# Kernel tuning notes

Measured on AMD Instinct MI355X. Metric: run time of the kernel, lower is better.

The kernel has to match this reference:

```python
import jax, jax.numpy as jnp
import numpy as np

INPUT_DIM = 41      # observed channels
D = 2 * INPUT_DIM   # attention value dim (values + mask concat)
E = 128             # embed_time
NH = 1              # num_heads
DK = E // NH
H = 128             # nhidden
NLIN = 50
LAT = 20
B, TK, TQ = 8, 512, 128


def _lin_init(k, out_d, in_d):
    return jax.random.normal(k, (out_d, in_d)) * (1.0 / np.sqrt(in_d))


def setup_inputs() -> dict:
    key = jax.random.key(0)
    ks = jax.random.split(key, 32)
    vals = jax.random.normal(ks[0], (B, TK, INPUT_DIM))
    obs = (jax.random.uniform(ks[1], (B, TK, INPUT_DIM)) > 0.3).astype(jnp.float32)
    x = jnp.concatenate([vals * obs, obs], axis=-1)          # [B,TK,2*INPUT_DIM]
    time_steps = jnp.sort(jax.random.uniform(ks[2], (B, TK)), axis=1)
    query = jnp.linspace(0.0, 1.0, TQ)                        # reference time points
    inp = dict(x=x, time_steps=time_steps, query=query)
    # learned time embedders (mtan_time_embedder): Linear(1,1) + Linear(1,E-1)
    inp['e1_wp'] = jax.random.normal(ks[3], (E - 1,)); inp['e1_bp'] = jax.random.normal(ks[4], (E - 1,)) * 0.1
    inp['e1_wl'] = jax.random.normal(ks[5], (1,));     inp['e1_bl'] = jax.random.normal(ks[6], (1,)) * 0.1
    inp['e2_wp'] = jax.random.normal(ks[7], (E - 1,)); inp['e2_bp'] = jax.random.normal(ks[8], (E - 1,)) * 0.1
    inp['e2_wl'] = jax.random.normal(ks[9], (1,));     inp['e2_bl'] = jax.random.normal(ks[10], (1,)) * 0.1
    # multiTimeAttention linears
    inp['Wq'] = _lin_init(ks[11], E, E); inp['bq'] = jnp.zeros((E,))
    inp['Wk'] = _lin_init(ks[12], E, E); inp['bk'] = jnp.zeros((E,))
    inp['Wo'] = _lin_init(ks[13], H, NH * D); inp['bo'] = jnp.zeros((H,))
    # bidirectional GRU (PyTorch layout: W_ih [3H,in], W_hh [3H,H])
    inp['gwi_f'] = _lin_init(ks[14], 3 * H, H); inp['gwh_f'] = _lin_init(ks[15], 3 * H, H)
    inp['gbi_f'] = jnp.zeros((3 * H,));         inp['gbh_f'] = jnp.zeros((3 * H,))
    inp['gwi_b'] = _lin_init(ks[16], 3 * H, H); inp['gwh_b'] = _lin_init(ks[17], 3 * H, H)
    inp['gbi_b'] = jnp.zeros((3 * H,));         inp['gbh_b'] = jnp.zeros((3 * H,))
    # hiddens_to_z0 MLP
    inp['W1'] = _lin_init(ks[18], NLIN, 2 * H); inp['b1'] = jnp.zeros((NLIN,))
    inp['W2'] = _lin_init(ks[19], 2 * LAT, NLIN); inp['b2'] = jnp.zeros((2 * LAT,))
    return inp


def _time_embed(tt, wp, bp, wl, bl):
    tt = tt[..., None]                               # [...,1]
    out1 = tt * wl + bl                              # [...,1]
    out2 = jnp.sin(tt * wp + bp)                     # [...,E-1]
    return jnp.concatenate([out1, out2], axis=-1)    # [...,E]


def _gru_scan(xs, Wi, Wh, bi, bh):
    # xs: [T,B,in] -> hidden states [T,B,H]; PyTorch GRU equations
    h0 = jnp.zeros((xs.shape[1], Wh.shape[1]), xs.dtype)
    def step(h, xt):
        gi = xt @ Wi.T + bi
        gh = h @ Wh.T + bh
        ir, iz, inn = jnp.split(gi, 3, axis=-1)
        hr, hz, hn = jnp.split(gh, 3, axis=-1)
        r = jax.nn.sigmoid(ir + hr)
        z = jax.nn.sigmoid(iz + hz)
        n = jnp.tanh(inn + r * hn)
        hnew = (1.0 - z) * n + z * h
        return hnew, hnew
    _, ys = jax.lax.scan(step, h0, xs)
    return ys


def reference(x, time_steps, query, e1_wp, e1_bp, e1_wl, e1_bl, e2_wp, e2_bp, e2_wl, e2_bl,
              Wq, bq, Wk, bk, Wo, bo, gwi_f, gwh_f, gbi_f, gbh_f, gwi_b, gwh_b, gbi_b, gbh_b,
              W1, b1, W2, b2):
    b, tk, _ = x.shape
    tq = query.shape[0]
    mask = x[:, :, INPUT_DIM:]                                 # [B,TK,INPUT_DIM]
    mask2 = jnp.concatenate([mask, mask], axis=-1)             # [B,TK,D]
    k_emb = _time_embed(time_steps, e1_wp, e1_bp, e1_wl, e1_bl)   # embedder1(key)   [B,TK,E]
    q_emb = _time_embed(query[None, :], e2_wp, e2_bp, e2_wl, e2_bl)  # embedder2(query) [1,TQ,E]
    q = (q_emb @ Wq.T + bq).reshape(1, tq, NH, DK).transpose(0, 2, 1, 3)   # [1,h,TQ,dk]
    k = (k_emb @ Wk.T + bk).reshape(b, tk, NH, DK).transpose(0, 2, 1, 3)   # [B,h,TK,dk]
    scores = jnp.einsum('ahqd,bhkd->bhqk', q, k) / np.sqrt(DK)             # [B,h,TQ,TK]
    # per-channel masked softmax over keys (the blown-up 5D tensor in the original)
    s5 = jnp.where(mask2[:, None, None, :, :] == 0, -1e9, scores[..., None])  # [B,h,TQ,TK,D]
    p = jax.nn.softmax(s5, axis=-2)
    att = jnp.einsum('bhqkd,bkd->bhqd', p, x)                  # value = x; [B,h,TQ,D]
    att = att.transpose(0, 2, 1, 3).reshape(b, tq, NH * D)
    out = att @ Wo.T + bo                                      # [B,TQ,H]
    xs = out.transpose(1, 0, 2)                                # [TQ,B,H]
    hf = _gru_scan(xs, gwi_f, gwh_f, gbi_f, gbh_f)
    hb = _gru_scan(xs[::-1], gwi_b, gwh_b, gbi_b, gbh_b)[::-1]
    h = jnp.concatenate([hf, hb], axis=-1).transpose(1, 0, 2)  # [B,TQ,2H]
    z = jax.nn.relu(h @ W1.T + b1) @ W2.T + b2                 # [B,TQ,2*LAT]
    return z
```

## Files before the change

kernel.cpp:

```cpp
#include <hip/hip_runtime.h>
#include <math.h>

#define TKK 512
#define TQQ 128
#define BB  8
#define EE  128
#define DD  82
#define IND 41
#define HH  128
#define G3  384
#define NL  50
#define OD  40

typedef __attribute__((ext_vector_type(8))) short short8v;
typedef __attribute__((ext_vector_type(4))) float f32x4;
#define MFMA16(a, b, c) __builtin_amdgcn_mfma_f32_16x16x32_bf16(a, b, c, 0, 0, 0)
#define RCP(x) __builtin_amdgcn_rcpf(x)

__device__ __forceinline__ short f2bf(float f) {
  unsigned u = __float_as_uint(f);
  unsigned r = (u + 0x7fffu + ((u >> 16) & 1u)) >> 16;
  return (short)r;
}
__device__ __forceinline__ float dot4(float4 a, float4 b) {
  return a.x * b.x + a.y * b.y + a.z * b.z + a.w * b.w;
}

__global__ __launch_bounds__(128) void embed_project(
    const float* __restrict__ time_steps, const float* __restrict__ query,
    const float* __restrict__ e1_wp, const float* __restrict__ e1_bp,
    const float* __restrict__ e1_wl, const float* __restrict__ e1_bl,
    const float* __restrict__ e2_wp, const float* __restrict__ e2_bp,
    const float* __restrict__ e2_wl, const float* __restrict__ e2_bl,
    const float* __restrict__ Wk, const float* __restrict__ bk,
    const float* __restrict__ Wq, const float* __restrict__ bq,
    float* __restrict__ kproj, float* __restrict__ qproj) {
  __shared__ float emb[8][EE];
  int i = blockIdx.x;
  int e = threadIdx.x;
  const float *wp, *bp, *wl, *bl, *W, *bias;
  float* out;
  int row0;
  const float* tsrc;
  if (i < 512) {
    int b = i & 7, rg = i >> 3;
    row0 = b * TKK + rg * 8;
    tsrc = time_steps + row0;
    wp = e1_wp; bp = e1_bp; wl = e1_wl; bl = e1_bl; W = Wk; bias = bk;
    out = kproj + (size_t)row0 * EE;
  } else {
    int qg = i - 512;
    row0 = qg * 8;
    tsrc = query + row0;
    wp = e2_wp; bp = e2_bp; wl = e2_wl; bl = e2_bl; W = Wq; bias = bq;
    out = qproj + (size_t)row0 * EE;
  }
  float wpv = 0.f, bpv = 0.f;
  if (e > 0) { wpv = wp[e - 1]; bpv = bp[e - 1]; }
  float wlv = wl[0], blv = bl[0];
#pragma unroll
  for (int r = 0; r < 8; r++) {
    float t = tsrc[r];
    emb[r][e] = (e == 0) ? (t * wlv + blv) : sinf(t * wpv + bpv);
  }
  __syncthreads();
  const float4* wr4 = (const float4*)(W + (size_t)e * EE);
  const float4* em4 = (const float4*)emb;
  float bv = bias[e];
  float acc[8];
#pragma unroll
  for (int r = 0; r < 8; r++) acc[r] = bv;
#pragma unroll 4
  for (int c = 0; c < 32; c++) {
    float4 wv = wr4[c];
#pragma unroll
    for (int r = 0; r < 8; r++) acc[r] += dot4(wv, em4[r * 32 + c]);
  }
#pragma unroll
  for (int r = 0; r < 8; r++) out[(size_t)r * EE + e] = acc[r];
}

__global__ __launch_bounds__(512) void attention(
    const float* __restrict__ x, const float* __restrict__ kproj,
    const float* __restrict__ qproj, const float* __restrict__ Wo,
    const float* __restrict__ bo,
    const float* __restrict__ gwi_f, const float* __restrict__ gbi_f,
    const float* __restrict__ gwi_b, const float* __restrict__ gbi_b,
    float* __restrict__ gi) {
  __shared__ float qv[4][EE];
  __shared__ float4 w4[TKK];
  __shared__ float red[8][4];
  __shared__ float mfin[4];
  __shared__ float part[4][4][DD];
  __shared__ float numb[4][DD];
  __shared__ float attb[4][DD];
  __shared__ float xsr[4][EE];
  __shared__ float wo_lds[HH * DD];
  int b = blockIdx.x & 7, qg = blockIdx.x >> 3;
  int q0 = qg * 4;
  int tid = threadIdx.x;
  int rq = tid >> 2, ec = tid & 3;

  {
    qv[tid >> 7][tid & 127] = qproj[(size_t)(q0 + (tid >> 7)) * EE + (tid & 127)];
    const float4* wo4 = (const float4*)Wo;
    float4* wl4 = (float4*)wo_lds;
#pragma unroll
    for (int it = 0; it < 6; it++) {
      int i4 = tid + it * 512;
      if (i4 < HH * DD / 4) wl4[i4] = wo4[i4];
    }
  }
  __syncthreads();

  const float scale = 0.08838834764831845f;
  float lm[4] = {-1e30f, -1e30f, -1e30f, -1e30f};
  const float4* qv4 = (const float4*)qv;
  for (int p = 0; p < 4; p++) {
    int r = p * 128 + rq;
    const float4* kr = (const float4*)(kproj + (size_t)(b * TKK + r) * EE);
    float s[4] = {0.f, 0.f, 0.f, 0.f};
#pragma unroll
    for (int c = 0; c < 8; c++) {
      float4 kv = kr[c * 4 + ec];
#pragma unroll
      for (int qi = 0; qi < 4; qi++) s[qi] += dot4(kv, qv4[qi * 32 + c * 4 + ec]);
    }
#pragma unroll
    for (int qi = 0; qi < 4; qi++) {
      s[qi] += __shfl_xor(s[qi], 1, 64);
      s[qi] += __shfl_xor(s[qi], 2, 64);
      s[qi] *= scale;
      lm[qi] = fmaxf(lm[qi], s[qi]);
    }
    if (ec == 0) { float4 sv = {s[0], s[1], s[2], s[3]}; w4[r] = sv; }
  }
  for (int off = 32; off; off >>= 1)
#pragma unroll
    for (int qi = 0; qi < 4; qi++) lm[qi] = fmaxf(lm[qi], __shfl_xor(lm[qi], off, 64));
  if ((tid & 63) == 0)
#pragma unroll
    for (int qi = 0; qi < 4; qi++) red[tid >> 6][qi] = lm[qi];
  __syncthreads();
  if (tid < 4) {
    float m = red[0][tid];
#pragma unroll
    for (int w = 1; w < 8; w++) m = fmaxf(m, red[w][tid]);
    mfin[tid] = m;
  }
  __syncthreads();
  {
    float m0 = mfin[0], m1 = mfin[1], m2 = mfin[2], m3 = mfin[3];
    float4 v0 = w4[tid];
    v0.x = __expf(v0.x - m0); v0.y = __expf(v0.y - m1);
    v0.z = __expf(v0.z - m2); v0.w = __expf(v0.w - m3);
    w4[tid] = v0;
  }
  __syncthreads();

  {
    int c2 = tid >> 7, d = tid & 127;
    if (d < DD) {
      const float* xp = x + ((size_t)(b * TKK + c2 * 128)) * DD + d;
      float a0 = 0.f, a1 = 0.f, a2 = 0.f, a3 = 0.f;
#pragma unroll 8
      for (int k = 0; k < 128; k++) {
        float xv = xp[(size_t)k * DD];
        float4 wv = w4[c2 * 128 + k];
        a0 += wv.x * xv; a1 += wv.y * xv; a2 += wv.z * xv; a3 += wv.w * xv;
      }
      part[c2][0][d] = a0; part[c2][1][d] = a1; part[c2][2][d] = a2; part[c2][3][d] = a3;
    }
  }
  __syncthreads();
  if (tid < DD) {
#pragma unroll
    for (int qi = 0; qi < 4; qi++)
      numb[qi][tid] = part[0][qi][tid] + part[1][qi][tid] + part[2][qi][tid] + part[3][qi][tid];
  }
  __syncthreads();
  if (tid < DD) {
    int j = tid % IND;
#pragma unroll
    for (int qi = 0; qi < 4; qi++)
      attb[qi][tid] = numb[qi][tid] * RCP(numb[qi][IND + j]);
  }
  __syncthreads();

  {
    int o = tid & 127, g = tid >> 7;
    const float* wrow = wo_lds + o * DD;
    float acc = bo[o];
#pragma unroll 2
    for (int d = 0; d < DD; d++) acc += wrow[d] * attb[g][d];
    xsr[g][o] = acc;
  }
  __syncthreads();

  const float4* xs4 = (const float4*)xsr;
  for (int p = 0; p < 6; p++) {
    int o = p * 128 + rq;
    int dirn = (o >= G3) ? 1 : 0;
    int oo = o - dirn * G3;
    int gate = oo >> 7, col = oo & 127;
    const float4* wr = (const float4*)((dirn ? gwi_b : gwi_f) + (size_t)oo * EE);
    float a[4] = {0.f, 0.f, 0.f, 0.f};
#pragma unroll
    for (int c = 0; c < 8; c++) {
      float4 wv = wr[c * 4 + ec];
#pragma unroll
      for (int qi = 0; qi < 4; qi++) a[qi] += dot4(wv, xs4[qi * 32 + c * 4 + ec]);
    }
#pragma unroll
    for (int qi = 0; qi < 4; qi++) {
      a[qi] += __shfl_xor(a[qi], 1, 64);
      a[qi] += __shfl_xor(a[qi], 2, 64);
    }
    float bi = (dirn ? gbi_b : gbi_f)[oo];
    if (ec == 0) {
      float* gp = gi + (((size_t)(dirn * BB + b) * TQQ + q0) * HH + col) * 4 + gate;
      gp[0] = a[0] + bi; gp[512] = a[1] + bi; gp[1024] = a[2] + bi; gp[1536] = a[3] + bi;
    }
  }
}

__global__ __launch_bounds__(256, 1) void gru_seq(const float* __restrict__ gi,
                                                  const float* __restrict__ gwh_f,
                                                  const float* __restrict__ gbh_f,
                                                  const float* __restrict__ gwh_b,
                                                  const float* __restrict__ gbh_b,
                                                  float* __restrict__ hcat) {
  __shared__ short hb[2][HH];
  int dir = blockIdx.x >> 3, b = blockIdx.x & 7;
  const float* Wh = dir ? gwh_b : gwh_f;
  const float* bh = dir ? gbh_b : gbh_f;
  int tid = threadIdx.x;
  int w = tid >> 6, l = tid & 63;
  int lhi = l >> 4, llo = l & 15;
  int col0 = 32 * w + llo, col1 = col0 + 16;
  bool c0 = (lhi < 2);
  int o_sel = c0 ? col0 : col1;
  bool wr_lane = ((lhi & 1) == 0);

  if (tid < HH) { hb[0][tid] = 0; hb[1][tid] = 0; }

  short8v Bf[2][3][4];
#pragma unroll
  for (int tj = 0; tj < 2; tj++) {
    int colt = 32 * w + 16 * tj + llo;
#pragma unroll
    for (int g = 0; g < 3; g++) {
      const float* wrp = Wh + (size_t)(g * HH + colt) * EE;
#pragma unroll
      for (int kk = 0; kk < 4; kk++) {
        int k0 = kk * 32 + lhi * 8;
        short8v v;
#pragma unroll
        for (int i = 0; i < 8; i++) v[i] = f2bf(wrp[k0 + i]);
        Bf[tj][g][kk] = v;
      }
    }
  }
  float bhr = bh[o_sel], bhz = bh[HH + o_sel], bhn = bh[2 * HH + o_sel];
  float hprev = 0.f;
  float hst[16];

  float4 g0, g1, g2, g3;
  const size_t dbase = ((size_t)(dir * BB + b) * TQQ) * 512 + (size_t)o_sel * 4;

  auto gi_load = [&](int step, float4& dst) {
    int tt = dir ? (TQQ - 1 - step) : step;
    dst = *(const float4*)(gi + dbase + (size_t)tt * 512);
  };
  __syncthreads();
  gi_load(0, g0); gi_load(1, g1); gi_load(2, g2);

  auto body = [&](int step, float4& gc, float4& gn, float& hs) {
    int cur = step & 1;
    const char* hrow = (const char*)&hb[cur][0];
    int ao = lhi * 16;
    short8v A0 = *(const short8v*)(hrow + 0 * 64 + ao);
    short8v A1 = *(const short8v*)(hrow + 1 * 64 + ao);
    short8v A2 = *(const short8v*)(hrow + 2 * 64 + ao);
    short8v A3 = *(const short8v*)(hrow + 3 * 64 + ao);
    { int ls = step + 3; gi_load(ls > TQQ - 1 ? TQQ - 1 : ls, gn); }
    f32x4 z4 = {0.f, 0.f, 0.f, 0.f};
    f32x4 aR0 = z4, aZ0 = z4, aN0 = z4, aR1 = z4, aZ1 = z4, aN1 = z4;
    aR0 = MFMA16(A0, Bf[0][0][0], aR0); aZ0 = MFMA16(A0, Bf[0][1][0], aZ0); aN0 = MFMA16(A0, Bf[0][2][0], aN0);
    aR1 = MFMA16(A0, Bf[1][0][0], aR1); aZ1 = MFMA16(A0, Bf[1][1][0], aZ1); aN1 = MFMA16(A0, Bf[1][2][0], aN1);
    aR0 = MFMA16(A1, Bf[0][0][1], aR0); aZ0 = MFMA16(A1, Bf[0][1][1], aZ0); aN0 = MFMA16(A1, Bf[0][2][1], aN0);
    aR1 = MFMA16(A1, Bf[1][0][1], aR1); aZ1 = MFMA16(A1, Bf[1][1][1], aZ1); aN1 = MFMA16(A1, Bf[1][2][1], aN1);
    aR0 = MFMA16(A2, Bf[0][0][2], aR0); aZ0 = MFMA16(A2, Bf[0][1][2], aZ0); aN0 = MFMA16(A2, Bf[0][2][2], aN0);
    aR1 = MFMA16(A2, Bf[1][0][2], aR1); aZ1 = MFMA16(A2, Bf[1][1][2], aZ1); aN1 = MFMA16(A2, Bf[1][2][2], aN1);
    aR0 = MFMA16(A3, Bf[0][0][3], aR0); aZ0 = MFMA16(A3, Bf[0][1][3], aZ0); aN0 = MFMA16(A3, Bf[0][2][3], aN0);
    aR1 = MFMA16(A3, Bf[1][0][3], aR1); aZ1 = MFMA16(A3, Bf[1][1][3], aZ1); aN1 = MFMA16(A3, Bf[1][2][3], aN1);
    float rs = c0 ? aR0[0] : aR1[0];
    float zs = c0 ? aZ0[0] : aZ1[0];
    float ns = c0 ? aN0[0] : aN1[0];
    float rp = gc.x + bhr + rs;
    float zp = gc.y + bhz + zs;
    float hn = ns + bhn;
    float r = RCP(1.f + __expf(-rp));
    float z = RCP(1.f + __expf(-zp));
    float a = gc.z + r * hn;
    float e = __expf(2.f * a);
    float n = 1.f - 2.f * RCP(1.f + e);
    float hnew = n + z * (hprev - n);
    hprev = hnew;
    hs = hnew;
    if (wr_lane) hb[cur ^ 1][o_sel] = f2bf(hnew);
    asm volatile("s_waitcnt lgkmcnt(0)" ::: "memory");
    __builtin_amdgcn_s_barrier();
    __builtin_amdgcn_sched_barrier(0);
  };

  for (int so = 0; so < TQQ / 16; so++) {
    int s0i = so * 16;
    body(s0i + 0,  g0, g3, hst[0]);
    body(s0i + 1,  g1, g0, hst[1]);
    body(s0i + 2,  g2, g1, hst[2]);
    body(s0i + 3,  g3, g2, hst[3]);
    body(s0i + 4,  g0, g3, hst[4]);
    body(s0i + 5,  g1, g0, hst[5]);
    body(s0i + 6,  g2, g1, hst[6]);
    body(s0i + 7,  g3, g2, hst[7]);
    body(s0i + 8,  g0, g3, hst[8]);
    body(s0i + 9,  g1, g0, hst[9]);
    body(s0i + 10, g2, g1, hst[10]);
    body(s0i + 11, g3, g2, hst[11]);
    body(s0i + 12, g0, g3, hst[12]);
    body(s0i + 13, g1, g0, hst[13]);
    body(s0i + 14, g2, g1, hst[14]);
    body(s0i + 15, g3, g2, hst[15]);
    if (wr_lane) {
#pragma unroll
      for (int si = 0; si < 16; si++) {
        int step = s0i + si;
        int t = dir ? (TQQ - 1 - step) : step;
        hcat[((size_t)b * TQQ + t) * (2 * HH) + dir * HH + o_sel] = hst[si];
      }
    }
  }
}

__global__ __launch_bounds__(512) void mlp_out(const float* __restrict__ hcat,
                                               const float* __restrict__ W1,
                                               const float* __restrict__ b1,
                                               const float* __restrict__ W2,
                                               const float* __restrict__ b2,
                                               float* __restrict__ out) {
  __shared__ float hrow[8][2 * HH];
  __shared__ float ybuf[8][52];
  int i = blockIdx.x;
  int b = i & 7, tg = i >> 3;
  int tid = threadIdx.x;
  size_t rowbase = (size_t)(b * TQQ + tg * 8) * (2 * HH);
  ((float4*)hrow)[tid] = *(const float4*)(hcat + rowbase + tid * 4);
  __syncthreads();
  int r = tid >> 6, o = tid & 63;
  if (o < NL) {
    const float4* w1 = (const float4*)(W1 + (size_t)o * (2 * HH));
    const float4* h4 = (const float4*)hrow[r];
    float acc = b1[o];
#pragma unroll 8
    for (int c = 0; c < 64; c++) acc += dot4(w1[c], h4[c]);
    ybuf[r][o] = fmaxf(acc, 0.f);
  }
  __syncthreads();
  if (o < OD) {
    const float* w2 = W2 + (size_t)o * NL;
    float acc = b2[o];
#pragma unroll 10
    for (int j = 0; j < NL; j++) acc += w2[j] * ybuf[r][j];
    out[((size_t)(b * TQQ + tg * 8) + r) * OD + o] = acc;
  }
}

extern "C" void kernel_launch(void* const* d_in, const int* in_sizes, int n_in,
                              void* d_out, int out_size, void* d_ws, size_t ws_size,
                              hipStream_t stream) {
  const float* x          = (const float*)d_in[0];
  const float* time_steps = (const float*)d_in[1];
  const float* query      = (const float*)d_in[2];
  const float* e1_wp = (const float*)d_in[3];
  const float* e1_bp = (const float*)d_in[4];
  const float* e1_wl = (const float*)d_in[5];
  const float* e1_bl = (const float*)d_in[6];
  const float* e2_wp = (const float*)d_in[7];
  const float* e2_bp = (const float*)d_in[8];
  const float* e2_wl = (const float*)d_in[9];
  const float* e2_bl = (const float*)d_in[10];
  const float* Wq = (const float*)d_in[11];
  const float* bq = (const float*)d_in[12];
  const float* Wk = (const float*)d_in[13];
  const float* bk = (const float*)d_in[14];
  const float* Wo = (const float*)d_in[15];
  const float* bo = (const float*)d_in[16];
  const float* gwi_f = (const float*)d_in[17];
  const float* gwh_f = (const float*)d_in[18];
  const float* gbi_f = (const float*)d_in[19];
  const float* gbh_f = (const float*)d_in[20];
  const float* gwi_b = (const float*)d_in[21];
  const float* gwh_b = (const float*)d_in[22];
  const float* gbi_b = (const float*)d_in[23];
  const float* gbh_b = (const float*)d_in[24];
  const float* W1 = (const float*)d_in[25];
  const float* b1 = (const float*)d_in[26];
  const float* W2 = (const float*)d_in[27];
  const float* b2 = (const float*)d_in[28];

  float* ws    = (float*)d_ws;
  float* kproj = ws;
  float* qproj = kproj + 4096 * 128;
  float* gi    = qproj + 128 * 128;
  float* hcat  = gi + 16 * 128 * 128 * 4;

  embed_project<<<528, 128, 0, stream>>>(time_steps, query,
                                         e1_wp, e1_bp, e1_wl, e1_bl,
                                         e2_wp, e2_bp, e2_wl, e2_bl,
                                         Wk, bk, Wq, bq, kproj, qproj);
  attention<<<256, 512, 0, stream>>>(x, kproj, qproj, Wo, bo,
                                     gwi_f, gbi_f, gwi_b, gbi_b, gi);
  gru_seq<<<16, 256, 0, stream>>>(gi, gwh_f, gbh_f, gwh_b, gbh_b, hcat);
  mlp_out<<<128, 512, 0, stream>>>(hcat, W1, b1, W2, b2, (float*)d_out);
}
```

Before: 99.84 us.

## Process eight queries per attention block and split GRU MFMA accumulation chains

Each attention block now handles eight query rows instead of four, so grid size halves. Each block then reuses its loaded key rows, x values, Wo tile and GRU input weights across twice as many queries, which cuts global and LDS traffic per query. The trade-off is fewer blocks on a large GPU, with more registers and LDS per block. Separately, the GRU recurrence splits each gate's four dependent MFMAs into two independent accumulator chains that are summed at the end, shortening the serial dependency latency on every time step.

New measurement: 165.2 us. 1.65x slower.

```diff
diff --git a/kernel.cpp b/kernel.cpp
--- a/kernel.cpp
+++ b/kernel.cpp
@@ -87,22 +87,26 @@
     const float* __restrict__ gwi_f, const float* __restrict__ gbi_f,
     const float* __restrict__ gwi_b, const float* __restrict__ gbi_b,
     float* __restrict__ gi) {
-  __shared__ float qv[4][EE];
-  __shared__ float4 w4[TKK];
-  __shared__ float red[8][4];
-  __shared__ float mfin[4];
-  __shared__ float part[4][4][DD];
-  __shared__ float numb[4][DD];
-  __shared__ float attb[4][DD];
-  __shared__ float xsr[4][EE];
+  __shared__ float qv[8][EE];
+  __shared__ float4 w8[TKK][2];
+  __shared__ float red[8][8];
+  __shared__ float mfin[8];
+  __shared__ float part[4][8][DD];
+  __shared__ float numb[8][DD];
+  __shared__ float attb[8][DD];
+  __shared__ float xsr[8][EE];
   __shared__ float wo_lds[HH * DD];
   int b = blockIdx.x & 7, qg = blockIdx.x >> 3;
-  int q0 = qg * 4;
+  int q0 = qg * 8;
   int tid = threadIdx.x;
   int rq = tid >> 2, ec = tid & 3;
 
   {
-    qv[tid >> 7][tid & 127] = qproj[(size_t)(q0 + (tid >> 7)) * EE + (tid & 127)];
+#pragma unroll
+    for (int it = 0; it < 2; it++) {
+      int idx = tid + it * 512;
+      qv[idx >> 7][idx & 127] = qproj[(size_t)(q0 + (idx >> 7)) * EE + (idx & 127)];
+    }
     const float4* wo4 = (const float4*)Wo;
     float4* wl4 = (float4*)wo_lds;
 #pragma unroll
@@ -114,35 +118,41 @@
   __syncthreads();
 
   const float scale = 0.08838834764831845f;
-  float lm[4] = {-1e30f, -1e30f, -1e30f, -1e30f};
+  float lm[8];
+#pragma unroll
+  for (int qi = 0; qi < 8; qi++) lm[qi] = -1e30f;
   const float4* qv4 = (const float4*)qv;
   for (int p = 0; p < 4; p++) {
     int r = p * 128 + rq;
     const float4* kr = (const float4*)(kproj + (size_t)(b * TKK + r) * EE);
-    float s[4] = {0.f, 0.f, 0.f, 0.f};
+    float s[8] = {0.f, 0.f, 0.f, 0.f, 0.f, 0.f, 0.f, 0.f};
 #pragma unroll
     for (int c = 0; c < 8; c++) {
       float4 kv = kr[c * 4 + ec];
 #pragma unroll
-      for (int qi = 0; qi < 4; qi++) s[qi] += dot4(kv, qv4[qi * 32 + c * 4 + ec]);
-    }
-#pragma unroll
-    for (int qi = 0; qi < 4; qi++) {
+      for (int qi = 0; qi < 8; qi++) s[qi] += dot4(kv, qv4[qi * 32 + c * 4 + ec]);
+    }
+#pragma unroll
+    for (int qi = 0; qi < 8; qi++) {
       s[qi] += __shfl_xor(s[qi], 1, 64);
       s[qi] += __shfl_xor(s[qi], 2, 64);
       s[qi] *= scale;
       lm[qi] = fmaxf(lm[qi], s[qi]);
     }
-    if (ec == 0) { float4 sv = {s[0], s[1], s[2], s[3]}; w4[r] = sv; }
+    if (ec == 0) {
+      float4 sv0 = {s[0], s[1], s[2], s[3]};
+      float4 sv1 = {s[4], s[5], s[6], s[7]};
+      w8[r][0] = sv0; w8[r][1] = sv1;
+    }
   }
   for (int off = 32; off; off >>= 1)
 #pragma unroll
-    for (int qi = 0; qi < 4; qi++) lm[qi] = fmaxf(lm[qi], __shfl_xor(lm[qi], off, 64));
+    for (int qi = 0; qi < 8; qi++) lm[qi] = fmaxf(lm[qi], __shfl_xor(lm[qi], off, 64));
   if ((tid & 63) == 0)
 #pragma unroll
-    for (int qi = 0; qi < 4; qi++) red[tid >> 6][qi] = lm[qi];
-  __syncthreads();
-  if (tid < 4) {
+    for (int qi = 0; qi < 8; qi++) red[tid >> 6][qi] = lm[qi];
+  __syncthreads();
+  if (tid < 8) {
     float m = red[0][tid];
 #pragma unroll
     for (int w = 1; w < 8; w++) m = fmaxf(m, red[w][tid]);
@@ -150,11 +160,12 @@
   }
   __syncthreads();
   {
-    float m0 = mfin[0], m1 = mfin[1], m2 = mfin[2], m3 = mfin[3];
-    float4 v0 = w4[tid];
-    v0.x = __expf(v0.x - m0); v0.y = __expf(v0.y - m1);
-    v0.z = __expf(v0.z - m2); v0.w = __expf(v0.w - m3);
-    w4[tid] = v0;
+    float4 v0 = w8[tid][0], v1 = w8[tid][1];
+    v0.x = __expf(v0.x - mfin[0]); v0.y = __expf(v0.y - mfin[1]);
+    v0.z = __expf(v0.z - mfin[2]); v0.w = __expf(v0.w - mfin[3]);
+    v1.x = __expf(v1.x - mfin[4]); v1.y = __expf(v1.y - mfin[5]);
+    v1.z = __expf(v1.z - mfin[6]); v1.w = __expf(v1.w - mfin[7]);
+    w8[tid][0] = v0; w8[tid][1] = v1;
   }
   __syncthreads();
 
@@ -162,27 +173,29 @@
     int c2 = tid >> 7, d = tid & 127;
     if (d < DD) {
       const float* xp = x + ((size_t)(b * TKK + c2 * 128)) * DD + d;
-      float a0 = 0.f, a1 = 0.f, a2 = 0.f, a3 = 0.f;
-#pragma unroll 8
+      float a[8] = {0.f, 0.f, 0.f, 0.f, 0.f, 0.f, 0.f, 0.f};
+#pragma unroll 4
       for (int k = 0; k < 128; k++) {
         float xv = xp[(size_t)k * DD];
-        float4 wv = w4[c2 * 128 + k];
-        a0 += wv.x * xv; a1 += wv.y * xv; a2 += wv.z * xv; a3 += wv.w * xv;
+        float4 w0 = w8[c2 * 128 + k][0], w1 = w8[c2 * 128 + k][1];
+        a[0] += w0.x * xv; a[1] += w0.y * xv; a[2] += w0.z * xv; a[3] += w0.w * xv;
+        a[4] += w1.x * xv; a[5] += w1.y * xv; a[6] += w1.z * xv; a[7] += w1.w * xv;
       }
-      part[c2][0][d] = a0; part[c2][1][d] = a1; part[c2][2][d] = a2; part[c2][3][d] = a3;
+#pragma unroll
+      for (int qi = 0; qi < 8; qi++) part[c2][qi][d] = a[qi];
     }
   }
   __syncthreads();
   if (tid < DD) {
 #pragma unroll
-    for (int qi = 0; qi < 4; qi++)
+    for (int qi = 0; qi < 8; qi++)
       numb[qi][tid] = part[0][qi][tid] + part[1][qi][tid] + part[2][qi][tid] + part[3][qi][tid];
   }
   __syncthreads();
   if (tid < DD) {
     int j = tid % IND;
 #pragma unroll
-    for (int qi = 0; qi < 4; qi++)
+    for (int qi = 0; qi < 8; qi++)
       attb[qi][tid] = numb[qi][tid] * RCP(numb[qi][IND + j]);
   }
   __syncthreads();
@@ -190,10 +203,15 @@
   {
     int o = tid & 127, g = tid >> 7;
     const float* wrow = wo_lds + o * DD;
-    float acc = bo[o];
+    float acc0 = bo[o], acc1 = acc0;
 #pragma unroll 2
-    for (int d = 0; d < DD; d++) acc += wrow[d] * attb[g][d];
-    xsr[g][o] = acc;
+    for (int d = 0; d < DD; d++) {
+      float wv = wrow[d];
+      acc0 += wv * attb[2 * g][d];
+      acc1 += wv * attb[2 * g + 1][d];
+    }
+    xsr[2 * g][o] = acc0;
+    xsr[2 * g + 1][o] = acc1;
   }
   __syncthreads();
 
@@ -204,22 +222,23 @@
     int oo = o - dirn * G3;
     int gate = oo >> 7, col = oo & 127;
     const float4* wr = (const float4*)((dirn ? gwi_b : gwi_f) + (size_t)oo * EE);
-    float a[4] = {0.f, 0.f, 0.f, 0.f};
+    float a[8] = {0.f, 0.f, 0.f, 0.f, 0.f, 0.f, 0.f, 0.f};
 #pragma unroll
     for (int c = 0; c < 8; c++) {
       float4 wv = wr[c * 4 + ec];
 #pragma unroll
-      for (int qi = 0; qi < 4; qi++) a[qi] += dot4(wv, xs4[qi * 32 + c * 4 + ec]);
-    }
-#pragma unroll
-    for (int qi = 0; qi < 4; qi++) {
+      for (int qi = 0; qi < 8; qi++) a[qi] += dot4(wv, xs4[qi * 32 + c * 4 + ec]);
+    }
+#pragma unroll
+    for (int qi = 0; qi < 8; qi++) {
       a[qi] += __shfl_xor(a[qi], 1, 64);
       a[qi] += __shfl_xor(a[qi], 2, 64);
     }
     float bi = (dirn ? gbi_b : gbi_f)[oo];
     if (ec == 0) {
       float* gp = gi + (((size_t)(dirn * BB + b) * TQQ + q0) * HH + col) * 4 + gate;
-      gp[0] = a[0] + bi; gp[512] = a[1] + bi; gp[1024] = a[2] + bi; gp[1536] = a[3] + bi;
+#pragma unroll
+      for (int qi = 0; qi < 8; qi++) gp[qi * 512] = a[qi] + bi;
     }
   }
 }
@@ -285,18 +304,19 @@
     short8v A3 = *(const short8v*)(hrow + 3 * 64 + ao);
     { int ls = step + 3; gi_load(ls > TQQ - 1 ? TQQ - 1 : ls, gn); }
     f32x4 z4 = {0.f, 0.f, 0.f, 0.f};
-    f32x4 aR0 = z4, aZ0 = z4, aN0 = z4, aR1 = z4, aZ1 = z4, aN1 = z4;
-    aR0 = MFMA16(A0, Bf[0][0][0], aR0); aZ0 = MFMA16(A0, Bf[0][1][0], aZ0); aN0 = MFMA16(A0, Bf[0][2][0], aN0);
-    aR1 = MFMA16(A0, Bf[1][0][0], aR1); aZ1 = MFMA16(A0, Bf[1][1][0], aZ1); aN1 = MFMA16(A0, Bf[1][2][0], aN1);
-    aR0 = MFMA16(A1, Bf[0][0][1], aR0); aZ0 = MFMA16(A1, Bf[0][1][1], aZ0); aN0 = MFMA16(A1, Bf[0][2][1], aN0);
-    aR1 = MFMA16(A1, Bf[1][0][1], aR1); aZ1 = MFMA16(A1, Bf[1][1][1], aZ1); aN1 = MFMA16(A1, Bf[1][2][1], aN1);
-    aR0 = MFMA16(A2, Bf[0][0][2], aR0); aZ0 = MFMA16(A2, Bf[0][1][2], aZ0); aN0 = MFMA16(A2, Bf[0][2][2], aN0);
-    aR1 = MFMA16(A2, Bf[1][0][2], aR1); aZ1 = MFMA16(A2, Bf[1][1][2], aZ1); aN1 = MFMA16(A2, Bf[1][2][2], aN1);
-    aR0 = MFMA16(A3, Bf[0][0][3], aR0); aZ0 = MFMA16(A3, Bf[0][1][3], aZ0); aN0 = MFMA16(A3, Bf[0][2][3], aN0);
-    aR1 = MFMA16(A3, Bf[1][0][3], aR1); aZ1 = MFMA16(A3, Bf[1][1][3], aZ1); aN1 = MFMA16(A3, Bf[1][2][3], aN1);
-    float rs = c0 ? aR0[0] : aR1[0];
-    float zs = c0 ? aZ0[0] : aZ1[0];
-    float ns = c0 ? aN0[0] : aN1[0];
+    f32x4 R0a = z4, R0b = z4, Z0a = z4, Z0b = z4, N0a = z4, N0b = z4;
+    f32x4 R1a = z4, R1b = z4, Z1a = z4, Z1b = z4, N1a = z4, N1b = z4;
+    R0a = MFMA16(A0, Bf[0][0][0], R0a); Z0a = MFMA16(A0, Bf[0][1][0], Z0a); N0a = MFMA16(A0, Bf[0][2][0], N0a);
+    R1a = MFMA16(A0, Bf[1][0][0], R1a); Z1a = MFMA16(A0, Bf[1][1][0], Z1a); N1a = MFMA16(A0, Bf[1][2][0], N1a);
+    R0b = MFMA16(A1, Bf[0][0][1], R0b); Z0b = MFMA16(A1, Bf[0][1][1], Z0b); N0b = MFMA16(A1, Bf[0][2][1], N0b);
+    R1b = MFMA16(A1, Bf[1][0][1], R1b); Z1b = MFMA16(A1, Bf[1][1][1], Z1b); N1b = MFMA16(A1, Bf[1][2][1], N1b);
+    R0a = MFMA16(A2, Bf[0][0][2], R0a); Z0a = MFMA16(A2, Bf[0][1][2], Z0a); N0a = MFMA16(A2, Bf[0][2][2], N0a);
+    R1a = MFMA16(A2, Bf[1][0][2], R1a); Z1a = MFMA16(A2, Bf[1][1][2], Z1a); N1a = MFMA16(A2, Bf[1][2][2], N1a);
+    R0b = MFMA16(A3, Bf[0][0][3], R0b); Z0b = MFMA16(A3, Bf[0][1][3], Z0b); N0b = MFMA16(A3, Bf[0][2][3], N0b);
+    R1b = MFMA16(A3, Bf[1][0][3], R1b); Z1b = MFMA16(A3, Bf[1][1][3], Z1b); N1b = MFMA16(A3, Bf[1][2][3], N1b);
+    float rs = c0 ? (R0a[0] + R0b[0]) : (R1a[0] + R1b[0]);
+    float zs = c0 ? (Z0a[0] + Z0b[0]) : (Z1a[0] + Z1b[0]);
+    float ns = c0 ? (N0a[0] + N0b[0]) : (N1a[0] + N1b[0]);
     float rp = gc.x + bhr + rs;
     float zp = gc.y + bhz + zs;
     float hn = ns + bhn;
@@ -419,7 +439,7 @@
                                          e1_wp, e1_bp, e1_wl, e1_bl,
                                          e2_wp, e2_bp, e2_wl, e2_bl,
                                          Wk, bk, Wq, bq, kproj, qproj);
-  attention<<<256, 512, 0, stream>>>(x, kproj, qproj, Wo, bo,
+  attention<<<128, 512, 0, stream>>>(x, kproj, qproj, Wo, bo,
                                      gwi_f, gbi_f, gwi_b, gbi_b, gi);
   gru_seq<<<16, 256, 0, stream>>>(gi, gwh_f, gbh_f, gwh_b, gbh_b, hcat);
   mlp_out<<<128, 512, 0, stream>>>(hcat, W1, b1, W2, b2, (float*)d_out);
```

## Split GRU input projection into separate kernel and break MFMA accumulator chains

Applied to the files above, without the earlier changes.

The GRU input-gate GEMM moves out of the attention kernel into its own gi_gemm kernel, which processes 8 query rows per block instead of 4 and so reuses each loaded weight row across twice as many outputs. Attention now writes its output projection to a workspace buffer. In the GRU recurrence, each gate's MFMA accumulation is split into two independent chains that are summed at the end, shortening the serial dependency on the critical sequential path. The cost is an extra kernel launch and a global round-trip for the intermediate xs.

New measurement: 126.5 us. 26.7% more time.

```diff
diff --git a/kernel.cpp b/kernel.cpp
--- a/kernel.cpp
+++ b/kernel.cpp
@@ -83,10 +83,7 @@
 __global__ __launch_bounds__(512) void attention(
     const float* __restrict__ x, const float* __restrict__ kproj,
     const float* __restrict__ qproj, const float* __restrict__ Wo,
-    const float* __restrict__ bo,
-    const float* __restrict__ gwi_f, const float* __restrict__ gbi_f,
-    const float* __restrict__ gwi_b, const float* __restrict__ gbi_b,
-    float* __restrict__ gi) {
+    const float* __restrict__ bo, float* __restrict__ xs) {
   __shared__ float qv[4][EE];
   __shared__ float4 w4[TKK];
   __shared__ float red[8][4];
@@ -94,7 +91,6 @@
   __shared__ float part[4][4][DD];
   __shared__ float numb[4][DD];
   __shared__ float attb[4][DD];
-  __shared__ float xsr[4][EE];
   __shared__ float wo_lds[HH * DD];
   int b = blockIdx.x & 7, qg = blockIdx.x >> 3;
   int q0 = qg * 4;
@@ -193,33 +189,53 @@
     float acc = bo[o];
 #pragma unroll 2
     for (int d = 0; d < DD; d++) acc += wrow[d] * attb[g][d];
-    xsr[g][o] = acc;
-  }
-  __syncthreads();
-
-  const float4* xs4 = (const float4*)xsr;
+    xs[((size_t)(q0 + g) * BB + b) * EE + o] = acc;
+  }
+}
+
+__global__ __launch_bounds__(512) void gi_gemm(
+    const float* __restrict__ xs,
+    const float* __restrict__ gwi_f, const float* __restrict__ gbi_f,
+    const float* __restrict__ gwi_b, const float* __restrict__ gbi_b,
+    float* __restrict__ gi) {
+  __shared__ float xsl[8][EE];
+  int b = blockIdx.x & 7, qh = blockIdx.x >> 3;
+  int q0 = qh * 8;
+  int tid = threadIdx.x;
+  int rq = tid >> 2, ec = tid & 3;
+
+  {
+    int r = tid >> 6, j = tid & 63;
+    const float* src = xs + ((size_t)(q0 + r) * BB + b) * EE;
+    xsl[r][j] = src[j];
+    xsl[r][j + 64] = src[j + 64];
+  }
+  __syncthreads();
+
+  const float4* xs4 = (const float4*)xsl;
   for (int p = 0; p < 6; p++) {
     int o = p * 128 + rq;
     int dirn = (o >= G3) ? 1 : 0;
     int oo = o - dirn * G3;
     int gate = oo >> 7, col = oo & 127;
     const float4* wr = (const float4*)((dirn ? gwi_b : gwi_f) + (size_t)oo * EE);
-    float a[4] = {0.f, 0.f, 0.f, 0.f};
+    float a[8] = {0.f, 0.f, 0.f, 0.f, 0.f, 0.f, 0.f, 0.f};
 #pragma unroll
     for (int c = 0; c < 8; c++) {
       float4 wv = wr[c * 4 + ec];
 #pragma unroll
-      for (int qi = 0; qi < 4; qi++) a[qi] += dot4(wv, xs4[qi * 32 + c * 4 + ec]);
-    }
-#pragma unroll
-    for (int qi = 0; qi < 4; qi++) {
+      for (int qi = 0; qi < 8; qi++) a[qi] += dot4(wv, xs4[qi * 32 + c * 4 + ec]);
+    }
+#pragma unroll
+    for (int qi = 0; qi < 8; qi++) {
       a[qi] += __shfl_xor(a[qi], 1, 64);
       a[qi] += __shfl_xor(a[qi], 2, 64);
     }
     float bi = (dirn ? gbi_b : gbi_f)[oo];
     if (ec == 0) {
       float* gp = gi + (((size_t)(dirn * BB + b) * TQQ + q0) * HH + col) * 4 + gate;
-      gp[0] = a[0] + bi; gp[512] = a[1] + bi; gp[1024] = a[2] + bi; gp[1536] = a[3] + bi;
+#pragma unroll
+      for (int qi = 0; qi < 8; qi++) gp[qi * 512] = a[qi] + bi;
     }
   }
 }
@@ -285,18 +301,19 @@
     short8v A3 = *(const short8v*)(hrow + 3 * 64 + ao);
     { int ls = step + 3; gi_load(ls > TQQ - 1 ? TQQ - 1 : ls, gn); }
     f32x4 z4 = {0.f, 0.f, 0.f, 0.f};
-    f32x4 aR0 = z4, aZ0 = z4, aN0 = z4, aR1 = z4, aZ1 = z4, aN1 = z4;
-    aR0 = MFMA16(A0, Bf[0][0][0], aR0); aZ0 = MFMA16(A0, Bf[0][1][0], aZ0); aN0 = MFMA16(A0, Bf[0][2][0], aN0);
-    aR1 = MFMA16(A0, Bf[1][0][0], aR1); aZ1 = MFMA16(A0, Bf[1][1][0], aZ1); aN1 = MFMA16(A0, Bf[1][2][0], aN1);
-    aR0 = MFMA16(A1, Bf[0][0][1], aR0); aZ0 = MFMA16(A1, Bf[0][1][1], aZ0); aN0 = MFMA16(A1, Bf[0][2][1], aN0);
-    aR1 = MFMA16(A1, Bf[1][0][1], aR1); aZ1 = MFMA16(A1, Bf[1][1][1], aZ1); aN1 = MFMA16(A1, Bf[1][2][1], aN1);
-    aR0 = MFMA16(A2, Bf[0][0][2], aR0); aZ0 = MFMA16(A2, Bf[0][1][2], aZ0); aN0 = MFMA16(A2, Bf[0][2][2], aN0);
-    aR1 = MFMA16(A2, Bf[1][0][2], aR1); aZ1 = MFMA16(A2, Bf[1][1][2], aZ1); aN1 = MFMA16(A2, Bf[1][2][2], aN1);
-    aR0 = MFMA16(A3, Bf[0][0][3], aR0); aZ0 = MFMA16(A3, Bf[0][1][3], aZ0); aN0 = MFMA16(A3, Bf[0][2][3], aN0);
-    aR1 = MFMA16(A3, Bf[1][0][3], aR1); aZ1 = MFMA16(A3, Bf[1][1][3], aZ1); aN1 = MFMA16(A3, Bf[1][2][3], aN1);
-    float rs = c0 ? aR0[0] : aR1[0];
-    float zs = c0 ? aZ0[0] : aZ1[0];
-    float ns = c0 ? aN0[0] : aN1[0];
+    f32x4 R0a = z4, R0b = z4, Z0a = z4, Z0b = z4, N0a = z4, N0b = z4;
+    f32x4 R1a = z4, R1b = z4, Z1a = z4, Z1b = z4, N1a = z4, N1b = z4;
+    R0a = MFMA16(A0, Bf[0][0][0], R0a); Z0a = MFMA16(A0, Bf[0][1][0], Z0a); N0a = MFMA16(A0, Bf[0][2][0], N0a);
+    R1a = MFMA16(A0, Bf[1][0][0], R1a); Z1a = MFMA16(A0, Bf[1][1][0], Z1a); N1a = MFMA16(A0, Bf[1][2][0], N1a);
+    R0b = MFMA16(A1, Bf[0][0][1], R0b); Z0b = MFMA16(A1, Bf[0][1][1], Z0b); N0b = MFMA16(A1, Bf[0][2][1], N0b);
+    R1b = MFMA16(A1, Bf[1][0][1], R1b); Z1b = MFMA16(A1, Bf[1][1][1], Z1b); N1b = MFMA16(A1, Bf[1][2][1], N1b);
+    R0a = MFMA16(A2, Bf[0][0][2], R0a); Z0a = MFMA16(A2, Bf[0][1][2], Z0a); N0a = MFMA16(A2, Bf[0][2][2], N0a);
+    R1a = MFMA16(A2, Bf[1][0][2], R1a); Z1a = MFMA16(A2, Bf[1][1][2], Z1a); N1a = MFMA16(A2, Bf[1][2][2], N1a);
+    R0b = MFMA16(A3, Bf[0][0][3], R0b); Z0b = MFMA16(A3, Bf[0][1][3], Z0b); N0b = MFMA16(A3, Bf[0][2][3], N0b);
+    R1b = MFMA16(A3, Bf[1][0][3], R1b); Z1b = MFMA16(A3, Bf[1][1][3], Z1b); N1b = MFMA16(A3, Bf[1][2][3], N1b);
+    float rs = c0 ? (R0a[0] + R0b[0]) : (R1a[0] + R1b[0]);
+    float zs = c0 ? (Z0a[0] + Z0b[0]) : (Z1a[0] + Z1b[0]);
+    float ns = c0 ? (N0a[0] + N0b[0]) : (N1a[0] + N1b[0]);
     float rp = gc.x + bhr + rs;
     float zp = gc.y + bhz + zs;
     float hn = ns + bhn;
@@ -412,15 +429,16 @@
   float* ws    = (float*)d_ws;
   float* kproj = ws;
   float* qproj = kproj + 4096 * 128;
-  float* gi    = qproj + 128 * 128;
+  float* xs    = qproj + 128 * 128;
+  float* gi    = xs + 128 * 8 * 128;
   float* hcat  = gi + 16 * 128 * 128 * 4;
 
   embed_project<<<528, 128, 0, stream>>>(time_steps, query,
                                          e1_wp, e1_bp, e1_wl, e1_bl,
                                          e2_wp, e2_bp, e2_wl, e2_bl,
                                          Wk, bk, Wq, bq, kproj, qproj);
-  attention<<<256, 512, 0, stream>>>(x, kproj, qproj, Wo, bo,
-                                     gwi_f, gbi_f, gwi_b, gbi_b, gi);
+  attention<<<256, 512, 0, stream>>>(x, kproj, qproj, Wo, bo, xs);
+  gi_gemm<<<128, 512, 0, stream>>>(xs, gwi_f, gbi_f, gwi_b, gbi_b, gi);
   gru_seq<<<16, 256, 0, stream>>>(gi, gwh_f, gbh_f, gwh_b, gbh_b, hcat);
   mlp_out<<<128, 512, 0, stream>>>(hcat, W1, b1, W2, b2, (float*)d_out);
 }
```
